# Optimization experiments

Measured on AMD Instinct MI355X. Metric: run time of the kernel, lower is better.

Reference implementation:

```python
import jax, jax.numpy as jnp
import numpy as np

B, H, W = 64, 128, 128
PS, G = 8, 16            # patch size, token grid (128//8)
E = 256                  # embed_dim (hidden_dim)
NS, IT, TEMP = 8, 3, 1.0 # num_slots, slot_iters, slot_temperature
V = 10                   # vocab_size
FD = 320                 # full_dim = latent_dim(256) + pose_dim(64)
HEADS, HD = 4, E // 4    # RoPE attn heads / head_dim
N = G * G


def _ln(x, g, b, eps=1e-5):
    m = x.mean(-1, keepdims=True)
    v = ((x - m) ** 2).mean(-1, keepdims=True)
    return (x - m) * jax.lax.rsqrt(v + eps) * g + b


def _conv(x, w, stride):
    return jax.lax.conv_general_dilated(
        x, w, (stride, stride), 'VALID',
        dimension_numbers=('NCHW', 'OIHW', 'NCHW'))


def _rope_tables(g, hd):
    half = hd // 2
    inv = 1.0 / (10000.0 ** (jnp.arange(0, half, 2, dtype=jnp.float32) / half))
    pos = jnp.arange(g, dtype=jnp.float32)
    p = jnp.outer(pos, inv)                                  # [g, half//2]
    e = jnp.concatenate([jnp.sin(p), jnp.cos(p)], axis=-1)   # [g, half]
    ex = jnp.broadcast_to(e[None, :, :], (g, g, half))
    ey = jnp.broadcast_to(e[:, None, :], (g, g, half))
    emb = jnp.concatenate([ey, ex], axis=-1).reshape(g * g, hd)
    return jnp.cos(emb)[None, :, None, :], jnp.sin(emb)[None, :, None, :]


def _apply_rope(x, cos, sin):
    x1, x2 = x[..., 0::2], x[..., 1::2]
    rot = jnp.concatenate([-x2, x1], axis=-1)
    return x * cos + rot * sin


def _gru(x, h, wih, whh, bih, bhh):
    gi = x @ wih.T + bih
    gh = h @ whh.T + bhh
    i_r, i_z, i_n = jnp.split(gi, 3, axis=-1)
    h_r, h_z, h_n = jnp.split(gh, 3, axis=-1)
    r = jax.nn.sigmoid(i_r + h_r)
    z = jax.nn.sigmoid(i_z + h_z)
    n = jnp.tanh(i_n + r * h_n)
    return (1.0 - z) * n + z * h


def setup_inputs() -> dict:
    key = jax.random.key(0)
    ks = iter(jax.random.split(key, 40))

    def nrm(shape, s=0.02):
        return (jax.random.normal(next(ks), shape, jnp.float32) * s)

    state = jax.random.randint(next(ks), (B, 1, H, W), 0, V).astype(jnp.float32)
    return {
        'state': state,
        'conv_w': nrm((E, 12, PS, PS)), 'conv_b': jnp.zeros((E,), jnp.float32),
        'mlp_ln_g': jnp.ones((E,), jnp.float32), 'mlp_ln_b': jnp.zeros((E,), jnp.float32),
        'mlp_w1': nrm((2 * E, E)), 'mlp_b1': jnp.zeros((2 * E,), jnp.float32),
        'mlp_w2': nrm((E, 2 * E)), 'mlp_b2': jnp.zeros((E,), jnp.float32),
        'qkv_w': nrm((3 * E, E)), 'qkv_b': jnp.zeros((3 * E,), jnp.float32),
        'proj_w': nrm((E, E)), 'proj_b': jnp.zeros((E,), jnp.float32),
        'ni_g': jnp.ones((E,), jnp.float32), 'ni_b': jnp.zeros((E,), jnp.float32),
        'ns_g': jnp.ones((FD,), jnp.float32), 'ns_b': jnp.zeros((FD,), jnp.float32),
        'nm_g': jnp.ones((FD,), jnp.float32), 'nm_b': jnp.zeros((FD,), jnp.float32),
        'q_w': nrm((FD, FD)), 'k_w': nrm((FD, E)), 'v_w': nrm((FD, E)),
        'gru_wih': nrm((3 * FD, FD)), 'gru_whh': nrm((3 * FD, FD)),
        'gru_bih': jnp.zeros((3 * FD,), jnp.float32), 'gru_bhh': jnp.zeros((3 * FD,), jnp.float32),
        'smlp_w1': nrm((2 * FD, FD)), 'smlp_b1': jnp.zeros((2 * FD,), jnp.float32),
        'smlp_w2': nrm((FD, 2 * FD)), 'smlp_b2': jnp.zeros((FD,), jnp.float32),
    }


def reference(state, conv_w, conv_b, mlp_ln_g, mlp_ln_b, mlp_w1, mlp_b1,
              mlp_w2, mlp_b2, qkv_w, qkv_b, proj_w, proj_b, ni_g, ni_b,
              ns_g, ns_b, nm_g, nm_b, q_w, k_w, v_w,
              gru_wih, gru_whh, gru_bih, gru_bhh,
              smlp_w1, smlp_b1, smlp_w2, smlp_b2):
    # Sobel edge features on replicate-padded image
    sob_x = jnp.array([[-1., 0., 1.], [-2., 0., 2.], [-1., 0., 1.]], jnp.float32).reshape(1, 1, 3, 3)
    sob_y = jnp.array([[-1., -2., -1.], [0., 0., 0.], [1., 2., 1.]], jnp.float32).reshape(1, 1, 3, 3)
    pad = jnp.pad(state, ((0, 0), (0, 0), (1, 1), (1, 1)), mode='edge')
    sx = _conv(pad, sob_x, 1)
    sy = _conv(pad, sob_y, 1)
    ids = jax.lax.stop_gradient(state)[:, 0].astype(jnp.int32)
    onehot = jax.nn.one_hot(ids, V, dtype=jnp.float32).transpose(0, 3, 1, 2)
    comp = jnp.concatenate([onehot, sx, sy], axis=1)            # [B,12,H,W]

    # Patch embed -> tokens [B,N,E]
    x = _conv(comp, conv_w, PS) + conv_b[None, :, None, None]   # [B,E,G,G]
    x = x.reshape(B, E, N).transpose(0, 2, 1)

    # patch_mlp (LN -> Linear -> GELU -> Linear), no residual
    h = _ln(x, mlp_ln_g, mlp_ln_b)
    h = jax.nn.gelu(h @ mlp_w1.T + mlp_b1, approximate=False)
    x = h @ mlp_w2.T + mlp_b2

    # RoPE self-attention, residual
    cos, sin = _rope_tables(G, HD)
    qkv = (x @ qkv_w.T + qkv_b).reshape(B, N, 3, HEADS, HD)
    q, k, v = qkv[:, :, 0], qkv[:, :, 1], qkv[:, :, 2]          # [B,N,Hh,HD]
    q = _apply_rope(q, cos, sin).transpose(0, 2, 1, 3)          # [B,Hh,N,HD]
    k = _apply_rope(k, cos, sin).transpose(0, 2, 1, 3)
    v = v.transpose(0, 2, 1, 3)
    attn = jax.nn.softmax(jnp.einsum('bhnd,bhmd->bhnm', q, k) * HD ** -0.5, axis=-1)
    ao = jnp.einsum('bhnm,bhmd->bhnd', attn, v).transpose(0, 2, 1, 3).reshape(B, N, E)
    x = x + (ao @ proj_w.T + proj_b)
    x = _ln(x, ni_g, ni_b)

    k_in = x @ k_w.T                                            # [B,N,FD]
    v_in = x @ v_w.T

    # No codebook injected -> zero slot priors
    slots = jnp.zeros((B, NS, FD), jnp.float32)
    sattn = None
    for _ in range(IT):
        slots_prev = slots
        q_s = _ln(slots, ns_g, ns_b) @ q_w.T                    # [B,NS,FD]
        logits = jnp.einsum('bnf,bsf->bns', k_in, q_s) * FD ** -0.5
        sattn = jax.nn.softmax(logits / TEMP, axis=-1)          # over slots
        an = sattn + 1e-8
        an = an / an.sum(axis=1, keepdims=True)                 # normalize over keys
        updates = jnp.einsum('bns,bnf->bsf', an, v_in)          # [B,NS,FD]
        slots = _gru(updates.reshape(-1, FD), slots_prev.reshape(-1, FD),
                     gru_wih, gru_whh, gru_bih, gru_bhh).reshape(B, NS, FD)
        m = _ln(slots, nm_g, nm_b)
        m = jax.nn.gelu(m @ smlp_w1.T + smlp_b1, approximate=False)
        slots = slots + (m @ smlp_w2.T + smlp_b2)

    masks = jax.lax.stop_gradient(sattn).transpose(0, 2, 1).reshape(B, NS, G, G)
    return slots, masks
```

## Files before the change

### kernel.cpp

```cpp
#include <hip/hip_runtime.h>
#include <math.h>

#define BB   64
#define HH   128
#define WW   128
#define GG   16
#define NN   256
#define EE   256
#define FD   320
#define NSL  8
#define NHEAD 4
#define HD   64
#define KIM  768

using short8 = __attribute__((ext_vector_type(8))) short;
using f32x4  = __attribute__((ext_vector_type(4))) float;

__device__ __forceinline__ float sigm(float x) { return 1.0f / (1.0f + expf(-x)); }
__device__ __forceinline__ float gelu_exact(float x) {
    return 0.5f * x * (1.0f + erff(x * 0.70710678118654752f));
}
__device__ __forceinline__ unsigned short f2b(float x) {
    unsigned u = __float_as_uint(x);
    u += 0x7fffu + ((u >> 16) & 1u);
    return (unsigned short)(u >> 16);
}
__device__ __forceinline__ float b2f(unsigned short u) {
    return __uint_as_float(((unsigned)u) << 16);
}
__device__ __forceinline__ void gload_lds16(const void* g, void* lds) {
    __builtin_amdgcn_global_load_lds(
        (const __attribute__((address_space(1))) unsigned int*)g,
        (__attribute__((address_space(3))) unsigned int*)lds, 16, 0, 0);
}
__device__ __forceinline__ void store_el(float* p, float v) { *p = v; }
__device__ __forceinline__ void store_el(unsigned short* p, float v) { *p = f2b(v); }
__device__ __forceinline__ float load_el(const float* p) { return *p; }
__device__ __forceinline__ float load_el(const unsigned short* p) { return b2f(*p); }

__global__ __launch_bounds__(256) void prep_all(
    const float* __restrict__ w0, const float* __restrict__ w1,
    const float* __restrict__ w2, const float* __restrict__ w3,
    const float* __restrict__ w4, const float* __restrict__ w5,
    const float* __restrict__ w6, const float* __restrict__ w7,
    const float* __restrict__ w8, const float* __restrict__ w9,
    const float* __restrict__ w10, const float* __restrict__ w11,
    unsigned short* __restrict__ dst,
    float* __restrict__ cs, float* __restrict__ sn,
    const float* __restrict__ state, unsigned short* __restrict__ X0) {
    int i = blockIdx.x * 256 + threadIdx.x;
    if (i < 2011136) {
        float v;
        if      (i <  196608) v = w0[i];
        else if (i <  327680) v = w1[i - 196608];
        else if (i <  458752) v = w2[i - 327680];
        else if (i <  655360) v = w3[i - 458752];
        else if (i <  720896) v = w4[i - 655360];
        else if (i <  802816) v = w5[i - 720896];
        else if (i <  884736) v = w6[i - 802816];
        else if (i <  987136) v = w7[i - 884736];
        else if (i < 1294336) v = w8[i - 987136];
        else if (i < 1601536) v = w9[i - 1294336];
        else if (i < 1806336) v = w10[i - 1601536];
        else                  v = w11[i - 1806336];
        dst[i] = f2b(v);
    } else if (i < 2027520) {
        int t = i - 2011136;
        int d = t & 63, n = t >> 6;
        int pos = (d < 32) ? (n >> 4) : (n & 15);
        int j = d & 31;
        float freq = powf(10000.0f, -(float)(j & 15) / 16.0f);
        float p = (float)pos * freq;
        float ang = (j < 16) ? sinf(p) : cosf(p);
        cs[t] = cosf(ang);
        sn[t] = sinf(ang);
    } else {
        int idx = i - 2027520;
        int w = idx % WW;
        int h = (idx / WW) % HH;
        int b = idx / (HH * WW);
        const float* st = state + (long)b * HH * WW;
        auto at = [&](int y, int x) {
            y = min(max(y, 0), HH - 1);
            x = min(max(x, 0), WW - 1);
            return st[y * WW + x];
        };
        float v00 = at(h-1, w-1), v01 = at(h-1, w), v02 = at(h-1, w+1);
        float v10 = at(h,   w-1),                  v12 = at(h,   w+1);
        float v20 = at(h+1, w-1), v21 = at(h+1, w), v22 = at(h+1, w+1);
        float sx = (v02 - v00) + 2.0f * (v12 - v10) + (v22 - v20);
        float sy = (v20 - v00) + 2.0f * (v21 - v01) + (v22 - v02);
        int id = (int)st[h * WW + w];
        int gy = h >> 3, ii = h & 7, gx = w >> 3, jj = w & 7;
        long row = (long)b * NN + gy * GG + gx;
        unsigned short* xr = X0 + row * KIM + ii * 8 + jj;
#pragma unroll
        for (int c = 0; c < 10; c++) xr[c * 64] = (id == c) ? 0x3F80u : 0u;
        xr[10 * 64] = f2b(sx);
        xr[11 * 64] = f2b(sy);
    }
}

template <int BM, int BN, int ACT>
__global__ __launch_bounds__(256) void gemm_bf16(
    const unsigned short* __restrict__ A, const unsigned short* __restrict__ W,
    const float* __restrict__ bias, const unsigned short* __restrict__ resb,
    float* __restrict__ C, unsigned short* __restrict__ Cb,
    int K, long sA, long sW, long sC1, long sC2, int cdiv, int ldc, float scale)
{
    constexpr bool HALF = (BM == 128 && BN == 64);
    constexpr int WN = BN / 64;
    constexpr int MF = HALF ? 2 : 4;
    __shared__ __align__(16) unsigned short As[BM * 32];
    __shared__ __align__(16) unsigned short Bs[BN * 32];
    const int tid = threadIdx.x;
    const int w = tid >> 6, l = tid & 63;
    const int wrow0 = HALF ? w * 32 : (w / WN) * 64;
    const int wcol0 = HALF ? 0 : (w % WN) * 64;
    const int bz = blockIdx.z;
    const unsigned short* Ab = A + (long)bz * sA + (long)(blockIdx.y * BM) * K;
    const unsigned short* Wb = W + (long)bz * sW + (long)(blockIdx.x * BN) * K;
    const long offC = (long)(bz / cdiv) * sC1 + (long)(bz % cdiv) * sC2;

    const int rA  = l >> 2;
    const int swz = ((l & 3) ^ ((l >> 3) & 3)) * 8;

    f32x4 acc[MF][4] = {};

    for (int k0 = 0; k0 < K; k0 += 32) {
#pragma unroll
        for (int c = 0; c < BM / 64; c++) {
            const int chunk = w * (BM / 64) + c;
            gload_lds16(Ab + (long)(chunk * 16 + rA) * K + k0 + swz, (char*)As + chunk * 1024);
        }
#pragma unroll
        for (int c = 0; c < BN / 64; c++) {
            const int chunk = w * (BN / 64) + c;
            gload_lds16(Wb + (long)(chunk * 16 + rA) * K + k0 + swz, (char*)Bs + chunk * 1024);
        }
        __syncthreads();
        short8 af[MF], bfr[4];
#pragma unroll
        for (int m = 0; m < MF; m++) {
            const int row = wrow0 + m * 16 + (l & 15);
            const int byte = row * 64 + (((l >> 4) ^ ((row >> 1) & 3)) << 4);
            af[m] = *(const short8*)((const char*)As + byte);
        }
#pragma unroll
        for (int n = 0; n < 4; n++) {
            const int row = wcol0 + n * 16 + (l & 15);
            const int byte = row * 64 + (((l >> 4) ^ ((row >> 1) & 3)) << 4);
            bfr[n] = *(const short8*)((const char*)Bs + byte);
        }
#pragma unroll
        for (int m = 0; m < MF; m++)
#pragma unroll
            for (int n = 0; n < 4; n++)
                acc[m][n] = __builtin_amdgcn_mfma_f32_16x16x32_bf16(af[m], bfr[n], acc[m][n], 0, 0, 0);
        __syncthreads();
    }

    const int crow0 = blockIdx.y * BM + wrow0;
    const int ccol0 = blockIdx.x * BN + wcol0;
#pragma unroll
    for (int m = 0; m < MF; m++) {
#pragma unroll
        for (int n = 0; n < 4; n++) {
            const int row = crow0 + m * 16 + ((l >> 4) << 2);
            const int col = ccol0 + n * 16 + (l & 15);
#pragma unroll
            for (int r = 0; r < 4; r++) {
                float v = acc[m][n][r] * scale;
                if (bias) v += bias[col];
                if (ACT == 1) v = gelu_exact(v);
                const long idx = offC + (long)(row + r) * ldc + col;
                if (resb) v += b2f(resb[idx]);
                if (C)  C[idx] = v;
                if (Cb) Cb[idx] = f2b(v);
            }
        }
    }
}

template <int ACT>
__global__ __launch_bounds__(256) void gemm_bf16_s(
    const unsigned short* __restrict__ A, const unsigned short* __restrict__ W,
    const float* __restrict__ bias0, const float* __restrict__ bias1,
    const float* __restrict__ res,
    float* __restrict__ C, unsigned short* __restrict__ Cb,
    int K, int N, long sA, long sW, long sC, float scale)
{
    __shared__ __align__(16) unsigned short As[64 * 32];
    __shared__ __align__(16) unsigned short Bs[64 * 32];
    const int tid = threadIdx.x;
    const int w = tid >> 6, l = tid & 63;
    const int gw = l >> 4, l15 = l & 15;
    const int bz = blockIdx.z;
    const unsigned short* Ab = A + (long)bz * sA + (long)(blockIdx.y * 64) * K;
    const unsigned short* Wb = W + (long)bz * sW + (long)(blockIdx.x * 64) * K;
    const float* bias = (bz == 0) ? bias0 : bias1;
    const long offC = (long)bz * sC;

    const int rA  = l >> 2;
    const int swz = ((l & 3) ^ ((l >> 3) & 3)) * 8;

    f32x4 acc[4] = {};

    for (int k0 = 0; k0 < K; k0 += 32) {
        gload_lds16(Ab + (long)(w * 16 + rA) * K + k0 + swz, (char*)As + w * 1024);
        gload_lds16(Wb + (long)(w * 16 + rA) * K + k0 + swz, (char*)Bs + w * 1024);
        __syncthreads();
        short8 af[4];
#pragma unroll
        for (int m = 0; m < 4; m++) {
            const int row = m * 16 + l15;
            af[m] = *(const short8*)((const char*)As + row * 64 + ((gw ^ ((row >> 1) & 3)) << 4));
        }
        const int brow = w * 16 + l15;
        const short8 bf = *(const short8*)((const char*)Bs + brow * 64 + ((gw ^ ((brow >> 1) & 3)) << 4));
#pragma unroll
        for (int m = 0; m < 4; m++)
            acc[m] = __builtin_amdgcn_mfma_f32_16x16x32_bf16(af[m], bf, acc[m], 0, 0, 0);
        __syncthreads();
    }

    const int col = blockIdx.x * 64 + w * 16 + l15;
    const int row0 = blockIdx.y * 64;
#pragma unroll
    for (int m = 0; m < 4; m++) {
        const int row = row0 + m * 16 + (gw << 2);
#pragma unroll
        for (int r = 0; r < 4; r++) {
            float v = acc[m][r] * scale;
            if (bias) v += bias[col];
            if (ACT == 1) v = gelu_exact(v);
            const long idx = offC + (long)(row + r) * N + col;
            if (res) v += res[idx];
            if (C)  C[idx] = v;
            if (Cb) Cb[idx] = f2b(v);
        }
    }
}

template <typename IT, typename OT>
__global__ __launch_bounds__(256) void ln_rows(const IT* __restrict__ X,
                                               OT* __restrict__ Y,
                                               const float* __restrict__ g,
                                               const float* __restrict__ b,
                                               int rows, int D) {
    int gtid = blockIdx.x * 256 + threadIdx.x;
    int row = gtid >> 6;
    int lane = gtid & 63;
    if (row >= rows) return;
    const IT* x = X + (long)row * D;
    const int nv = D >> 6;
    float v[5];
    float s = 0.0f;
#pragma unroll 5
    for (int i = 0; i < nv; i++) { v[i] = load_el(&x[lane + (i << 6)]); s += v[i]; }
#pragma unroll
    for (int o = 32; o; o >>= 1) s += __shfl_down(s, o);
    s = __shfl(s, 0);
    float mean = s / (float)D;
    float s2 = 0.0f;
#pragma unroll 5
    for (int i = 0; i < nv; i++) { float d = v[i] - mean; s2 += d * d; }
#pragma unroll
    for (int o = 32; o; o >>= 1) s2 += __shfl_down(s2, o);
    s2 = __shfl(s2, 0);
    float inv = rsqrtf(s2 / (float)D + 1e-5f);
    OT* y = Y + (long)row * D;
#pragma unroll 5
    for (int i = 0; i < nv; i++) {
        int d = lane + (i << 6);
        store_el(&y[d], (v[i] - mean) * inv * g[d] + b[d]);
    }
}

__global__ __launch_bounds__(256) void gru_ln(const float* __restrict__ GI,
                                              const float* __restrict__ GH,
                                              float* __restrict__ slots,
                                              const float* __restrict__ g,
                                              const float* __restrict__ b,
                                              unsigned short* __restrict__ SLnb) {
    int gtid = blockIdx.x * 256 + threadIdx.x;
    int row = gtid >> 6;
    int lane = gtid & 63;
    const float* gi = GI + (long)row * 960;
    const float* gh = GH + (long)row * 960;
    float* sl = slots + (long)row * FD;
    float h[5];
    float s = 0.0f;
#pragma unroll
    for (int i = 0; i < 5; i++) {
        const int f = lane + (i << 6);
        const float rr = sigm(gi[f] + gh[f]);
        const float z  = sigm(gi[320 + f] + gh[320 + f]);
        const float nn = tanhf(gi[640 + f] + rr * gh[640 + f]);
        const float hn = (1.0f - z) * nn + z * sl[f];
        h[i] = hn;
        s += hn;
        sl[f] = hn;
    }
#pragma unroll
    for (int o = 32; o; o >>= 1) s += __shfl_down(s, o);
    s = __shfl(s, 0);
    const float mean = s * (1.0f / FD);
    float s2 = 0.0f;
#pragma unroll
    for (int i = 0; i < 5; i++) { const float d = h[i] - mean; s2 += d * d; }
#pragma unroll
    for (int o = 32; o; o >>= 1) s2 += __shfl_down(s2, o);
    s2 = __shfl(s2, 0);
    const float inv = rsqrtf(s2 * (1.0f / FD) + 1e-5f);
    unsigned short* y = SLnb + (long)row * FD;
#pragma unroll
    for (int i = 0; i < 5; i++) {
        const int f = lane + (i << 6);
        y[f] = f2b((h[i] - mean) * inv * g[f] + b[f]);
    }
}

__global__ __launch_bounds__(256) void rope_qk(const unsigned short* __restrict__ QKVb,
                                               const float* __restrict__ cs,
                                               const float* __restrict__ sn,
                                               unsigned short* __restrict__ Qr,
                                               unsigned short* __restrict__ Kr) {
    const int rid = blockIdx.x * 256 + threadIdx.x;
    const int n = rid & 255;
    const int h = (rid >> 8) & 3;
    const int b = rid >> 10;
    const unsigned short* src = QKVb + ((long)(b * 256 + n)) * 768 + h * 64;
    float cv[64], sv[64];
#pragma unroll
    for (int i = 0; i < 16; i++) {
        *(float4*)&cv[i * 4] = *(const float4*)(cs + n * 64 + i * 4);
        *(float4*)&sv[i * 4] = *(const float4*)(sn + n * 64 + i * 4);
    }
#pragma unroll
    for (int qk = 0; qk < 2; qk++) {
        const unsigned short* s0 = src + qk * 256;
        unsigned short* dst = (qk == 0 ? Qr : Kr) + (long)rid * 64;
        float x[64];
#pragma unroll
        for (int i = 0; i < 8; i++) {
            short8 v = *(const short8*)(s0 + i * 8);
#pragma unroll
            for (int j = 0; j < 8; j++) x[i * 8 + j] = b2f((unsigned short)v[j]);
        }
        unsigned short o[64];
#pragma unroll
        for (int d = 0; d < 64; d++) {
            const float rot = (d < 32) ? -x[2 * d + 1] : x[2 * (d - 32)];
            o[d] = f2b(x[d] * cv[d] + rot * sv[d]);
        }
#pragma unroll
        for (int i = 0; i < 8; i++)
            *(short8*)(dst + i * 8) = *(short8*)&o[i * 8];
    }
}

__global__ __launch_bounds__(256, 1) void fused_attn(
    const unsigned short* __restrict__ Qr,
    const unsigned short* __restrict__ Kr,
    const unsigned short* __restrict__ QKVb,
    unsigned short* __restrict__ AOb)
{
    __shared__ __align__(16) char SL[49152];
    const int h = blockIdx.x, b = blockIdx.y;
    const int p = blockIdx.z;
    const int tid = threadIdx.x;
    const int w = tid >> 6, l = tid & 63;
    const int gw = l >> 4, l15 = l & 15;
    const long bh = (long)b * 4 + h;
    const unsigned short* Qb = Qr + bh * NN * 64;
    const unsigned short* Kb = Kr + bh * NN * 64;

    {
        const int n0 = (tid & 127) * 2;
        const int dh = tid >> 7;
        const unsigned short* v0p = QKVb + ((long)b * NN + n0) * 768 + h * 64 + 512 + dh * 32;
        const unsigned short* v1p = v0p + 768;
        unsigned short v0[32], v1[32];
#pragma unroll
        for (int i = 0; i < 4; i++) {
            *(short8*)&v0[i * 8] = *(const short8*)(v0p + i * 8);
            *(short8*)&v1[i * 8] = *(const short8*)(v1p + i * 8);
        }
#pragma unroll
        for (int i = 0; i < 32; i++) {
            const int d = dh * 32 + i;
            const unsigned val = (unsigned)v0[i] | ((unsigned)v1[i] << 16);
            *(unsigned*)(SL + d * 512 + (((n0 >> 3) ^ (d & 15)) << 4) + (n0 & 7) * 2) = val;
        }
    }
    __syncthreads();

    char* Pw = SL + 32768 + w * 4096;

    {
        const int mbase = w * 64 + p * 32;
        f32x4 accs[16][2] = {};
#pragma unroll
        for (int kk = 0; kk < 2; kk++) {
            short8 bq[2];
#pragma unroll
            for (int mf = 0; mf < 2; mf++)
                bq[mf] = *(const short8*)(Qb + ((mbase + mf * 16 + l15) << 6) + kk * 32 + gw * 8);
#pragma unroll
            for (int nf = 0; nf < 16; nf++) {
                const short8 ak = *(const short8*)(Kb + ((nf * 16 + l15) << 6) + kk * 32 + gw * 8);
#pragma unroll
                for (int mf = 0; mf < 2; mf++)
                    accs[nf][mf] = __builtin_amdgcn_mfma_f32_16x16x32_bf16(ak, bq[mf], accs[nf][mf], 0, 0, 0);
            }
        }
        float rs[2];
#pragma unroll
        for (int mf = 0; mf < 2; mf++) {
            float mx = -1e30f;
#pragma unroll
            for (int nf = 0; nf < 16; nf++)
#pragma unroll
                for (int r = 0; r < 4; r++) mx = fmaxf(mx, accs[nf][mf][r]);
            mx = fmaxf(mx, __shfl_xor(mx, 16));
            mx = fmaxf(mx, __shfl_xor(mx, 32));
            float sum = 0.0f;
#pragma unroll
            for (int nf = 0; nf < 16; nf++)
#pragma unroll
                for (int r = 0; r < 4; r++) {
                    const float e = expf((accs[nf][mf][r] - mx) * 0.125f);
                    accs[nf][mf][r] = e;
                    sum += e;
                }
            sum += __shfl_xor(sum, 16);
            sum += __shfl_xor(sum, 32);
            rs[mf] = 1.0f / sum;
        }
        f32x4 acco[4][2] = {};
#pragma unroll
        for (int c = 0; c < 4; c++) {
#pragma unroll
            for (int nfi = 0; nfi < 4; nfi++) {
                const int nf = c * 4 + nfi;
                const int kt = nf >> 1;
                const int gr = (nf & 1) * 2 + (gw >> 1);
                const int lr = l15 + 16 * gr;
                const int j0 = (gw & 1) * 4;
#pragma unroll
                for (int mf = 0; mf < 2; mf++) {
                    uint2 pk;
                    pk.x = (unsigned)f2b(accs[nf][mf][0] * rs[mf]) |
                           ((unsigned)f2b(accs[nf][mf][1] * rs[mf]) << 16);
                    pk.y = (unsigned)f2b(accs[nf][mf][2] * rs[mf]) |
                           ((unsigned)f2b(accs[nf][mf][3] * rs[mf]) << 16);
                    *(uint2*)(Pw + ((kt & 1) * 2 + mf) * 1024 + lr * 16 + j0 * 2) = pk;
                }
            }
#pragma unroll
            for (int kti = 0; kti < 2; kti++) {
                const int kt = c * 2 + kti;
                short8 vf[4];
#pragma unroll
                for (int df = 0; df < 4; df++) {
                    const int d = df * 16 + l15;
                    vf[df] = *(const short8*)(SL + d * 512 + (((kt * 4 + gw) ^ (d & 15)) << 4));
                }
#pragma unroll
                for (int mf = 0; mf < 2; mf++) {
                    const short8 pf = *(const short8*)(Pw + (kti * 2 + mf) * 1024 + l * 16);
#pragma unroll
                    for (int df = 0; df < 4; df++)
                        acco[df][mf] = __builtin_amdgcn_mfma_f32_16x16x32_bf16(vf[df], pf, acco[df][mf], 0, 0, 0);
                }
            }
        }
#pragma unroll
        for (int df = 0; df < 4; df++)
#pragma unroll
            for (int mf = 0; mf < 2; mf++) {
                const int m = mbase + mf * 16 + l15;
                const int d = df * 16 + gw * 4;
                unsigned short o[4];
#pragma unroll
                for (int r = 0; r < 4; r++) o[r] = f2b(acco[df][mf][r]);
                *(uint2*)(AOb + ((long)(b * NN + m) * 256 + h * 64 + d)) = *(uint2*)o;
            }
    }
}

__global__ __launch_bounds__(256) void slot_logits(const unsigned short* __restrict__ KVin,
                                                   const float* __restrict__ Qs,
                                                   float* __restrict__ sattn,
                                                   float* __restrict__ sums2,
                                                   float* __restrict__ mout) {
    const int b = blockIdx.x;
    const int chunk = blockIdx.y;
    __shared__ float qs[NSL][FD];
    __shared__ float colsum[NSL];
    const int tid = threadIdx.x;
    for (int i = tid; i < NSL * FD; i += 256) qs[i / FD][i % FD] = Qs[(long)b * NSL * FD + i];
    if (tid < NSL) colsum[tid] = 0.0f;
    __syncthreads();
    const int wv = tid >> 6, lane = tid & 63;
    float wsum[NSL] = {};
#pragma unroll
    for (int rr = 0; rr < 4; rr++) {
        const int r = chunk * 16 + wv * 4 + rr;
        const unsigned short* kr = KVin + ((long)b * NN + r) * 640;
        float acc[NSL] = {};
#pragma unroll
        for (int i = 0; i < 5; i++) {
            const int t = lane + (i << 6);
            const float kv = b2f(kr[t]);
#pragma unroll
            for (int s = 0; s < NSL; s++) acc[s] = fmaf(kv, qs[s][t], acc[s]);
        }
#pragma unroll
        for (int s = 0; s < NSL; s++)
#pragma unroll
            for (int o = 32; o; o >>= 1) acc[s] += __shfl_down(acc[s], o);
        if (lane == 0) {
            const float scale = 0.055901699437494740f;
            float mx = -1e30f;
#pragma unroll
            for (int s = 0; s < NSL; s++) { acc[s] *= scale; mx = fmaxf(mx, acc[s]); }
            float e[NSL], sum = 0.0f;
#pragma unroll
            for (int s = 0; s < NSL; s++) { e[s] = expf(acc[s] - mx); sum += e[s]; }
            const float rsum = 1.0f / sum;
            float* outp = sattn + ((long)b * NN + r) * NSL;
#pragma unroll
            for (int s = 0; s < NSL; s++) {
                const float pp = e[s] * rsum;
                outp[s] = pp;
                wsum[s] += pp;
                if (mout) mout[(long)b * 2048 + s * 256 + r] = pp;
            }
        }
    }
    if (lane == 0) {
#pragma unroll
        for (int s = 0; s < NSL; s++) atomicAdd(&colsum[s], wsum[s]);
    }
    __syncthreads();
    if (tid < NSL) sums2[((long)(b << 4) + chunk) * NSL + tid] = colsum[tid];
}

__global__ __launch_bounds__(256) void slot_updates(const float* __restrict__ sattn,
                                                    const float* __restrict__ sums2,
                                                    const unsigned short* __restrict__ KVin,
                                                    unsigned short* __restrict__ Updb) {
    const int b = blockIdx.x;
    const int tid = threadIdx.x;
    const int w = tid >> 6, l = tid & 63;
    __shared__ float inv_s[NSL];
    __shared__ float an_s[NN][NSL];
    __shared__ float red[4][NSL][FD];
    if (tid < NSL) {
        float tot = (float)NN * 1e-8f;
#pragma unroll
        for (int c = 0; c < 16; c++) tot += sums2[((long)(b << 4) + c) * NSL + tid];
        inv_s[tid] = 1.0f / tot;
    }
    __syncthreads();
    {
        const float4 p0 = *(const float4*)(sattn + ((long)b * NN + tid) * NSL);
        const float4 p1 = *(const float4*)(sattn + ((long)b * NN + tid) * NSL + 4);
        an_s[tid][0] = (p0.x + 1e-8f) * inv_s[0];
        an_s[tid][1] = (p0.y + 1e-8f) * inv_s[1];
        an_s[tid][2] = (p0.z + 1e-8f) * inv_s[2];
        an_s[tid][3] = (p0.w + 1e-8f) * inv_s[3];
        an_s[tid][4] = (p1.x + 1e-8f) * inv_s[4];
        an_s[tid][5] = (p1.y + 1e-8f) * inv_s[5];
        an_s[tid][6] = (p1.z + 1e-8f) * inv_s[6];
        an_s[tid][7] = (p1.w + 1e-8f) * inv_s[7];
    }
    __syncthreads();
    float acc[NSL][5] = {};
    const unsigned short* vb = KVin + ((long)b * NN + w * 64) * 640 + 320;
    for (int i = 0; i < 64; i++) {
        float v[5];
#pragma unroll
        for (int j = 0; j < 5; j++) v[j] = b2f(vb[(long)i * 640 + l + (j << 6)]);
        float a[NSL];
#pragma unroll
        for (int s = 0; s < NSL; s++) a[s] = an_s[w * 64 + i][s];
#pragma unroll
        for (int s = 0; s < NSL; s++)
#pragma unroll
            for (int j = 0; j < 5; j++)
                acc[s][j] = fmaf(a[s], v[j], acc[s][j]);
    }
#pragma unroll
    for (int s = 0; s < NSL; s++)
#pragma unroll
        for (int j = 0; j < 5; j++)
            red[w][s][l + (j << 6)] = acc[s][j];
    __syncthreads();
    for (int idx = tid; idx < NSL * FD; idx += 256) {
        const int s = idx / FD, f = idx % FD;
        const float tot = red[0][s][f] + red[1][s][f] + red[2][s][f] + red[3][s][f];
        Updb[((long)b * NSL + s) * FD + f] = f2b(tot);
    }
}

extern "C" void kernel_launch(void* const* d_in, const int* in_sizes, int n_in,
                              void* d_out, int out_size, void* d_ws, size_t ws_size,
                              hipStream_t stream) {
    const float* state    = (const float*)d_in[0];
    const float* conv_w   = (const float*)d_in[1];
    const float* conv_b   = (const float*)d_in[2];
    const float* mlp_ln_g = (const float*)d_in[3];
    const float* mlp_ln_b = (const float*)d_in[4];
    const float* mlp_w1   = (const float*)d_in[5];
    const float* mlp_b1   = (const float*)d_in[6];
    const float* mlp_w2   = (const float*)d_in[7];
    const float* mlp_b2   = (const float*)d_in[8];
    const float* qkv_w    = (const float*)d_in[9];
    const float* qkv_b    = (const float*)d_in[10];
    const float* proj_w   = (const float*)d_in[11];
    const float* proj_b   = (const float*)d_in[12];
    const float* ni_g     = (const float*)d_in[13];
    const float* ni_b     = (const float*)d_in[14];
    const float* ns_g     = (const float*)d_in[15];
    const float* ns_b     = (const float*)d_in[16];
    const float* nm_g     = (const float*)d_in[17];
    const float* nm_b     = (const float*)d_in[18];
    const float* q_w      = (const float*)d_in[19];
    const float* k_w      = (const float*)d_in[20];
    const float* v_w      = (const float*)d_in[21];
    const float* gru_wih  = (const float*)d_in[22];
    const float* gru_whh  = (const float*)d_in[23];
    const float* gru_bih  = (const float*)d_in[24];
    const float* gru_bhh  = (const float*)d_in[25];
    const float* smlp_w1  = (const float*)d_in[26];
    const float* smlp_b1  = (const float*)d_in[27];
    const float* smlp_w2  = (const float*)d_in[28];
    const float* smlp_b2  = (const float*)d_in[29];

    float* ws = (float*)d_ws;
    const int M = BB * NN;
    typedef unsigned short u16;

    u16*   X0b  = (u16*)(ws + 0L);
    u16*   Qr   = (u16*)(ws + 0L);
    u16*   Kr   = (u16*)(ws + 2097152L);
    u16*   X1b  = (u16*)(ws + 6291456L);
    u16*   XLNb = (u16*)(ws + 10485760L);
    u16*   Hbufb= (u16*)(ws + 12582912L);
    u16*   QKVb = (u16*)(ws + 6291456L);
    u16*   X2b  = (u16*)(ws + 23068672L);
    u16*   X3b  = (u16*)(ws + 31457280L);
    u16*   Xnb  = (u16*)(ws + 33554432L);
    float* Slots= ws + 35651584L;
    float* Qs   = ws + 35979264L;
    float* Satt = ws + 36143104L;
    float* Sums2= ws + 36274176L;
    float* GI   = ws + 36438528L;
    float* GH   = ws + 36930048L;
    u16*   SLnb = (u16*)(ws + 37421568L);
    u16*   Updb = (u16*)(ws + 37503488L);
    u16*   Slotsb=(u16*)(ws + 37585408L);
    u16*   Mhb  = (u16*)(ws + 37667328L);
    u16*   KVinb= (u16*)(ws + 39845888L);
    u16*   AOb    = (u16*)(ws + 50331648L);
    u16*   wb     = (u16*)(ws + 52428800L);
    u16*   conv_wb= wb + 0;
    u16*   mlp_w1b= wb + 196608;
    u16*   mlp_w2b= wb + 327680;
    u16*   qkv_wb = wb + 458752;
    u16*   proj_wb= wb + 655360;
    u16*   kv_wb  = wb + 720896;
    u16*   q_wb   = wb + 884736;
    u16*   wihb   = wb + 987136;
    u16*   whhb   = wb + 1294336;
    u16*   smlp1b = wb + 1601536;
    u16*   smlp2b = wb + 1806336;
    float* CS     = ws + 53434368L;
    float* SN     = ws + 53450752L;

    float* out = (float*)d_out;

    auto gemmA = [&](const u16* A, const u16* Wt, const float* bias, const u16* resb,
                     float* C, u16* Cb, int Mm, int Nn, int Kk, int batch,
                     long sA, long sW, long sC1, long sC2, int cdiv, int ldc,
                     float scale, int act) {
        dim3 grid(Nn / 128, Mm / 128, batch);
        if (act) gemm_bf16<128, 128, 1><<<grid, 256, 0, stream>>>(A, Wt, bias, resb, C, Cb, Kk, sA, sW, sC1, sC2, cdiv, ldc, scale);
        else     gemm_bf16<128, 128, 0><<<grid, 256, 0, stream>>>(A, Wt, bias, resb, C, Cb, Kk, sA, sW, sC1, sC2, cdiv, ldc, scale);
    };
    auto gemmA64 = [&](const u16* A, const u16* Wt, const float* bias, const u16* resb,
                       float* C, u16* Cb, int Mm, int Nn, int Kk, int ldc) {
        dim3 grid(Nn / 64, Mm / 128, 1);
        gemm_bf16<128, 64, 0><<<grid, 256, 0, stream>>>(A, Wt, bias, resb, C, Cb, Kk, 0, 0, 0, 0, 1, ldc, 1.0f);
    };
    auto gemmB = [&](const u16* A, const u16* Wt, u16* Cb, int Mm, int Nn, int Kk) {
        dim3 grid(Nn / 64, Mm / 256, 1);
        gemm_bf16<256, 64, 0><<<grid, 256, 0, stream>>>(A, Wt, nullptr, nullptr, nullptr, Cb, Kk, 0, 0, 0, 0, 1, Nn, 1.0f);
    };
    auto gemmS = [&](const u16* A, const u16* Wt, const float* b0, const float* b1,
                     const float* res, float* C, u16* Cb, int Mm, int Nn, int Kk,
                     int batch, long sA, long sW, long sC, int act) {
        dim3 grid(Nn / 64, Mm / 64, batch);
        if (act) gemm_bf16_s<1><<<grid, 256, 0, stream>>>(A, Wt, b0, b1, res, C, Cb, Kk, Nn, sA, sW, sC, 1.0f);
        else     gemm_bf16_s<0><<<grid, 256, 0, stream>>>(A, Wt, b0, b1, res, C, Cb, Kk, Nn, sA, sW, sC, 1.0f);
    };

    prep_all<<<dim3(3076096 / 256), 256, 0, stream>>>(conv_w, mlp_w1, mlp_w2, qkv_w,
                                                      proj_w, k_w, v_w, q_w,
                                                      gru_wih, gru_whh, smlp_w1, smlp_w2,
                                                      wb, CS, SN, state, X0b);

    gemmA64(X0b, conv_wb, conv_b, nullptr, nullptr, X1b, M, EE, KIM, EE);
    ln_rows<<<dim3(M * 64 / 256), 256, 0, stream>>>(X1b, XLNb, mlp_ln_g, mlp_ln_b, M, EE);
    gemmA(XLNb, mlp_w1b, mlp_b1, nullptr, nullptr, Hbufb, M, 2 * EE, EE, 1, 0, 0, 0, 0, 1, 2 * EE, 1.0f, 1);
    gemmA64(Hbufb, mlp_w2b, mlp_b2, nullptr, nullptr, X2b, M, EE, 2 * EE, EE);
    gemmA(X2b, qkv_wb, qkv_b, nullptr, nullptr, QKVb, M, 3 * EE, EE, 1, 0, 0, 0, 0, 1, 3 * EE, 1.0f, 0);
    rope_qk<<<dim3(65536 / 256), 256, 0, stream>>>(QKVb, CS, SN, Qr, Kr);
    fused_attn<<<dim3(NHEAD, BB, 2), 256, 0, stream>>>(Qr, Kr, QKVb, AOb);
    gemmA64(AOb, proj_wb, proj_b, X2b, nullptr, X3b, M, EE, EE, EE);
    ln_rows<<<dim3(M * 64 / 256), 256, 0, stream>>>(X3b, Xnb, ni_g, ni_b, M, EE);
    gemmB(Xnb, kv_wb, KVinb, M, 640, EE);
    hipMemsetAsync(Slots, 0, (size_t)BB * NSL * FD * sizeof(float), stream);
    hipMemsetAsync(Slotsb, 0, (size_t)BB * NSL * FD * sizeof(u16), stream);
    for (int it = 0; it < 3; it++) {
        ln_rows<<<dim3(512 * 64 / 256), 256, 0, stream>>>(Slots, SLnb, ns_g, ns_b, 512, FD);
        gemmS(SLnb, q_wb, nullptr, nullptr, nullptr, Qs, nullptr, 512, FD, FD, 1, 0, 0, 0, 0);
        slot_logits<<<dim3(BB, 16), 256, 0, stream>>>(KVinb, Qs, Satt, Sums2,
                                                      (it == 2) ? (out + 163840) : nullptr);
        slot_updates<<<dim3(BB), 256, 0, stream>>>(Satt, Sums2, KVinb, Updb);
        gemmS(Updb, wihb, gru_bih, gru_bhh, nullptr, GI, nullptr, 512, 960, FD,
              2, 163840, 307200, 491520, 0);
        gru_ln<<<dim3(512 * 64 / 256), 256, 0, stream>>>(GI, GH, Slots, nm_g, nm_b, SLnb);
        gemmS(SLnb, smlp1b, smlp_b1, nullptr, nullptr, nullptr, Mhb, 512, 2 * FD, FD, 1, 0, 0, 0, 1);
        if (it < 2)
            gemmS(Mhb, smlp2b, smlp_b2, nullptr, Slots, Slots, Slotsb, 512, FD, 2 * FD, 1, 0, 0, 0, 0);
        else
            gemmS(Mhb, smlp2b, smlp_b2, nullptr, Slots, out, nullptr, 512, FD, 2 * FD, 1, 0, 0, 0, 0);
    }
}
```

Before: 583.8 us.

## Fuse RoPE into attention kernel and fold slot zeroing into prep kernel

Removes the standalone rope_qk kernel. Each attention block now loads the raw Q/K rows from the QKV buffer, applies the rotary embedding and writes the results into swizzled shared memory, which grows from 48KB to 96KB. The two memsets that zeroed the slot buffers are moved into extra threads of the prep kernel. This saves launches and the Q/K global round trip, but K RoPE is recomputed in both z-halves, and the larger LDS footprint with per-thread 64-element arrays may raise register pressure.

```diff
diff --git a/kernel.cpp b/kernel.cpp
--- a/kernel.cpp
+++ b/kernel.cpp
@@ -47,7 +47,8 @@
     const float* __restrict__ w10, const float* __restrict__ w11,
     unsigned short* __restrict__ dst,
     float* __restrict__ cs, float* __restrict__ sn,
-    const float* __restrict__ state, unsigned short* __restrict__ X0) {
+    const float* __restrict__ state, unsigned short* __restrict__ X0,
+    float* __restrict__ slots0, unsigned short* __restrict__ slotsb0) {
     int i = blockIdx.x * 256 + threadIdx.x;
     if (i < 2011136) {
         float v;
@@ -74,7 +75,7 @@
         float ang = (j < 16) ? sinf(p) : cosf(p);
         cs[t] = cosf(ang);
         sn[t] = sinf(ang);
-    } else {
+    } else if (i < 3076096) {
         int idx = i - 2027520;
         int w = idx % WW;
         int h = (idx / WW) % HH;
@@ -98,6 +99,10 @@
         for (int c = 0; c < 10; c++) xr[c * 64] = (id == c) ? 0x3F80u : 0u;
         xr[10 * 64] = f2b(sx);
         xr[11 * 64] = f2b(sy);
+    } else if (i < 3239936) {
+        slots0[i - 3076096] = 0.0f;
+    } else {
+        slotsb0[i - 3239936] = 0;
     }
 }
 
@@ -321,60 +326,17 @@
     }
 }
 
-__global__ __launch_bounds__(256) void rope_qk(const unsigned short* __restrict__ QKVb,
-                                               const float* __restrict__ cs,
-                                               const float* __restrict__ sn,
-                                               unsigned short* __restrict__ Qr,
-                                               unsigned short* __restrict__ Kr) {
-    const int rid = blockIdx.x * 256 + threadIdx.x;
-    const int n = rid & 255;
-    const int h = (rid >> 8) & 3;
-    const int b = rid >> 10;
-    const unsigned short* src = QKVb + ((long)(b * 256 + n)) * 768 + h * 64;
-    float cv[64], sv[64];
-#pragma unroll
-    for (int i = 0; i < 16; i++) {
-        *(float4*)&cv[i * 4] = *(const float4*)(cs + n * 64 + i * 4);
-        *(float4*)&sv[i * 4] = *(const float4*)(sn + n * 64 + i * 4);
-    }
-#pragma unroll
-    for (int qk = 0; qk < 2; qk++) {
-        const unsigned short* s0 = src + qk * 256;
-        unsigned short* dst = (qk == 0 ? Qr : Kr) + (long)rid * 64;
-        float x[64];
-#pragma unroll
-        for (int i = 0; i < 8; i++) {
-            short8 v = *(const short8*)(s0 + i * 8);
-#pragma unroll
-            for (int j = 0; j < 8; j++) x[i * 8 + j] = b2f((unsigned short)v[j]);
-        }
-        unsigned short o[64];
-#pragma unroll
-        for (int d = 0; d < 64; d++) {
-            const float rot = (d < 32) ? -x[2 * d + 1] : x[2 * (d - 32)];
-            o[d] = f2b(x[d] * cv[d] + rot * sv[d]);
-        }
-#pragma unroll
-        for (int i = 0; i < 8; i++)
-            *(short8*)(dst + i * 8) = *(short8*)&o[i * 8];
-    }
-}
-
 __global__ __launch_bounds__(256, 1) void fused_attn(
-    const unsigned short* __restrict__ Qr,
-    const unsigned short* __restrict__ Kr,
     const unsigned short* __restrict__ QKVb,
+    const float* __restrict__ cs, const float* __restrict__ sn,
     unsigned short* __restrict__ AOb)
 {
-    __shared__ __align__(16) char SL[49152];
+    __shared__ __align__(16) char SL[98304];
     const int h = blockIdx.x, b = blockIdx.y;
     const int p = blockIdx.z;
     const int tid = threadIdx.x;
     const int w = tid >> 6, l = tid & 63;
     const int gw = l >> 4, l15 = l & 15;
-    const long bh = (long)b * 4 + h;
-    const unsigned short* Qb = Qr + bh * NN * 64;
-    const unsigned short* Kb = Kr + bh * NN * 64;
 
     {
         const int n0 = (tid & 127) * 2;
@@ -394,22 +356,71 @@
             *(unsigned*)(SL + d * 512 + (((n0 >> 3) ^ (d & 15)) << 4) + (n0 & 7) * 2) = val;
         }
     }
+    {
+        const int n = tid;
+        const unsigned short* src = QKVb + ((long)(b * NN + n)) * 768 + h * 64 + 256;
+        float x[64];
+#pragma unroll
+        for (int i = 0; i < 8; i++) {
+            short8 v = *(const short8*)(src + i * 8);
+#pragma unroll
+            for (int j = 0; j < 8; j++) x[i * 8 + j] = b2f((unsigned short)v[j]);
+        }
+        unsigned short o[64];
+#pragma unroll
+        for (int d = 0; d < 64; d++) {
+            const float rot = (d < 32) ? -x[2 * d + 1] : x[2 * (d - 32)];
+            o[d] = f2b(x[d] * cs[n * 64 + d] + rot * sn[n * 64 + d]);
+        }
+        char* kb = SL + 32768 + n * 128;
+        const int xo = (n & 7) << 4;
+#pragma unroll
+        for (int i = 0; i < 8; i++)
+            *(short8*)(kb + ((i * 16) ^ xo)) = *(short8*)&o[i * 8];
+    }
+    if (tid < 128) {
+        const int r = tid;
+        const int gq = (r >> 5) * 64 + p * 32 + (r & 31);
+        const unsigned short* src = QKVb + ((long)(b * NN + gq)) * 768 + h * 64;
+        float x[64];
+#pragma unroll
+        for (int i = 0; i < 8; i++) {
+            short8 v = *(const short8*)(src + i * 8);
+#pragma unroll
+            for (int j = 0; j < 8; j++) x[i * 8 + j] = b2f((unsigned short)v[j]);
+        }
+        unsigned short o[64];
+#pragma unroll
+        for (int d = 0; d < 64; d++) {
+            const float rot = (d < 32) ? -x[2 * d + 1] : x[2 * (d - 32)];
+            o[d] = f2b(x[d] * cs[gq * 64 + d] + rot * sn[gq * 64 + d]);
+        }
+        char* qb = SL + 65536 + r * 128;
+        const int xo = (r & 7) << 4;
+#pragma unroll
+        for (int i = 0; i < 8; i++)
+            *(short8*)(qb + ((i * 16) ^ xo)) = *(short8*)&o[i * 8];
+    }
     __syncthreads();
 
-    char* Pw = SL + 32768 + w * 4096;
+    char* Pw = SL + 81920 + w * 4096;
 
     {
         const int mbase = w * 64 + p * 32;
         f32x4 accs[16][2] = {};
 #pragma unroll
         for (int kk = 0; kk < 2; kk++) {
+            const int cb = (kk * 64 + gw * 16);
             short8 bq[2];
 #pragma unroll
-            for (int mf = 0; mf < 2; mf++)
-                bq[mf] = *(const short8*)(Qb + ((mbase + mf * 16 + l15) << 6) + kk * 32 + gw * 8);
+            for (int mf = 0; mf < 2; mf++) {
+                const int r = w * 32 + mf * 16 + l15;
+                bq[mf] = *(const short8*)(SL + 65536 + r * 128 + (cb ^ ((r & 7) << 4)));
+            }
 #pragma unroll
             for (int nf = 0; nf < 16; nf++) {
-                const short8 ak = *(const short8*)(Kb + ((nf * 16 + l15) << 6) + kk * 32 + gw * 8);
+                const int n = nf * 16 + l15;
+                const short8 ak = *(const short8*)(SL + 32768 + n * 128 + (cb ^ ((n & 7) << 4)));
 #pragma unroll
                 for (int mf = 0; mf < 2; mf++)
                     accs[nf][mf] = __builtin_amdgcn_mfma_f32_16x16x32_bf16(ak, bq[mf], accs[nf][mf], 0, 0, 0);
@@ -645,8 +656,6 @@
     typedef unsigned short u16;
 
     u16*   X0b  = (u16*)(ws + 0L);
-    u16*   Qr   = (u16*)(ws + 0L);
-    u16*   Kr   = (u16*)(ws + 2097152L);
     u16*   X1b  = (u16*)(ws + 6291456L);
     u16*   XLNb = (u16*)(ws + 10485760L);
     u16*   Hbufb= (u16*)(ws + 12582912L);
@@ -708,23 +717,20 @@
         else     gemm_bf16_s<0><<<grid, 256, 0, stream>>>(A, Wt, b0, b1, res, C, Cb, Kk, Nn, sA, sW, sC, 1.0f);
     };
 
-    prep_all<<<dim3(3076096 / 256), 256, 0, stream>>>(conv_w, mlp_w1, mlp_w2, qkv_w,
+    prep_all<<<dim3(3403776 / 256), 256, 0, stream>>>(conv_w, mlp_w1, mlp_w2, qkv_w,
                                                       proj_w, k_w, v_w, q_w,
                                                       gru_wih, gru_whh, smlp_w1, smlp_w2,
-                                                      wb, CS, SN, state, X0b);
+                                                      wb, CS, SN, state, X0b, Slots, Slotsb);
 
     gemmA64(X0b, conv_wb, conv_b, nullptr, nullptr, X1b, M, EE, KIM, EE);
     ln_rows<<<dim3(M * 64 / 256), 256, 0, stream>>>(X1b, XLNb, mlp_ln_g, mlp_ln_b, M, EE);
     gemmA(XLNb, mlp_w1b, mlp_b1, nullptr, nullptr, Hbufb, M, 2 * EE, EE, 1, 0, 0, 0, 0, 1, 2 * EE, 1.0f, 1);
     gemmA64(Hbufb, mlp_w2b, mlp_b2, nullptr, nullptr, X2b, M, EE, 2 * EE, EE);
     gemmA(X2b, qkv_wb, qkv_b, nullptr, nullptr, QKVb, M, 3 * EE, EE, 1, 0, 0, 0, 0, 1, 3 * EE, 1.0f, 0);
-    rope_qk<<<dim3(65536 / 256), 256, 0, stream>>>(QKVb, CS, SN, Qr, Kr);
-    fused_attn<<<dim3(NHEAD, BB, 2), 256, 0, stream>>>(Qr, Kr, QKVb, AOb);
+    fused_attn<<<dim3(NHEAD, BB, 2), 256, 0, stream>>>(QKVb, CS, SN, AOb);
     gemmA64(AOb, proj_wb, proj_b, X2b, nullptr, X3b, M, EE, EE, EE);
     ln_rows<<<dim3(M * 64 / 256), 256, 0, stream>>>(X3b, Xnb, ni_g, ni_b, M, EE);
     gemmB(Xnb, kv_wb, KVinb, M, 640, EE);
-    hipMemsetAsync(Slots, 0, (size_t)BB * NSL * FD * sizeof(float), stream);
-    hipMemsetAsync(Slotsb, 0, (size_t)BB * NSL * FD * sizeof(u16), stream);
     for (int it = 0; it < 3; it++) {
         ln_rows<<<dim3(512 * 64 / 256), 256, 0, stream>>>(Slots, SLnb, ns_g, ns_b, 512, FD);
         gemmS(SLnb, q_wb, nullptr, nullptr, nullptr, Qs, nullptr, 512, FD, FD, 1, 0, 0, 0, 0);
```

Result: no change. 579.0 us (-0.8%).
